# Kernel optimization log

Hardware: AMD Instinct MI355X
Metric: run time of the kernel (lower is better)

The kernel has to match this reference:

```python
import jax, jax.numpy as jnp
import numpy as np

# ---- config (matches init_kwargs) ----
M, N, D = 8, 512, 243            # meshes, neurons per mesh, input dim
E_RATIO = 0.8
NE = int(N * E_RATIO)            # 409 excitatory
NI = N - NE                      # 103 inhibitory
TICKS = 16
BATCH = 512
BITS = 4
WSCALE = 8.0
VTH, VRESET = 1.0, 0.0
TAU_E, TAU_I, DT = 2.0, 1.5, 1.0
BETA = 10.0                      # fast-sigmoid surrogate slope
INPUT_SCALE = 1.0


def fake_quant(w):
    """Quantization-aware fake quant with straight-through estimator."""
    step = WSCALE / (2 ** (BITS - 1))          # 1.0 for 4-bit, scale 8
    q = jnp.clip(jnp.round(w / step), -(2 ** (BITS - 1)), 2 ** (BITS - 1) - 1) * step
    return w + jax.lax.stop_gradient(q - w)


@jax.custom_vjp
def spike(u):
    return (u >= 0.0).astype(u.dtype)

def _spike_fwd(u):
    return spike(u), u

def _spike_bwd(u, g):
    # fast-sigmoid surrogate gradient
    return (g * BETA / (1.0 + BETA * jnp.abs(u)) ** 2,)

spike.defvjp(_spike_fwd, _spike_bwd)


def setup_inputs() -> dict:
    key = jax.random.key(0)
    ks = jax.random.split(key, 8)

    def sparse_w(k, shape, density, std, zero_diag=False):
        km, kw = jax.random.split(k)
        mask = (jax.random.uniform(km, shape) < density).astype(jnp.float32)
        if zero_diag:
            mask = mask * (1.0 - jnp.eye(shape[-1], dtype=jnp.float32))
        return jax.random.normal(kw, shape) * std * mask

    x = jax.random.normal(ks[0], (BATCH, D), dtype=jnp.float32)
    W_in = jax.random.normal(ks[1], (M, N, D)) * 0.8      # per-mesh input projection [out,in]
    b_in = jax.random.normal(ks[2], (M, N)) * 0.05
    W_inter = sparse_w(ks[3], (M, N, NE), 0.3, 0.8)        # inter-mesh: E of mesh m -> mesh m+1
    W_EE = sparse_w(ks[4], (M, NE, NE), 0.5, 0.8, True)
    W_EI = sparse_w(ks[5], (M, NI, NE), 0.6, 0.8)
    W_IE = sparse_w(ks[6], (M, NE, NI), 0.8, 0.8)
    W_II = sparse_w(ks[7], (M, NI, NI), 0.7, 0.8, True)
    return dict(x=x, W_in=W_in, b_in=b_in, W_inter=W_inter,
                W_EE=W_EE, W_EI=W_EI, W_IE=W_IE, W_II=W_II)


def reference(x, W_in, b_in, W_inter, W_EE, W_EI, W_IE, W_II):
    B = x.shape[0]
    decay_E = 1.0 - DT / TAU_E
    decay_I = 1.0 - DT / TAU_I

    # quantize weights once (constant across ticks)
    qW_in, qW_inter = fake_quant(W_in), fake_quant(W_inter)
    qW_EE, qW_EI = fake_quant(W_EE), fake_quant(W_EI)
    qW_IE, qW_II = fake_quant(W_IE), fake_quant(W_II)

    # external input projection, same every tick: [M, B, N]
    ext_proj = jnp.einsum('bd,mnd->mbn', x * INPUT_SCALE, qW_in) + b_in[:, None, :]

    def tick(carry, _):
        e, i, vE, vI, acc = carry          # e:[M,B,NE] i:[M,B,NI]
        # inter-mesh: mesh m receives inter_connections[m-1](e_prev[m-1])
        inter = jnp.einsum('mbe,mne->mbn', e, qW_inter)
        ext = ext_proj + jnp.roll(inter, 1, axis=0)
        cE = ext[:, :, :NE] \
            + jnp.einsum('mbe,mfe->mbf', e, qW_EE) \
            + jnp.einsum('mbi,mfi->mbf', i, qW_IE)
        cI = ext[:, :, NE:] \
            + jnp.einsum('mbe,mfe->mbf', e, qW_EI) \
            + jnp.einsum('mbi,mfi->mbf', i, qW_II)
        # LIF: leaky decay + input, threshold, hard reset
        vE = vE * decay_E + cE * DT
        vI = vI * decay_I + cI * DT
        sE = spike(vE - VTH)
        sI = spike(vI - VTH)
        vE = sE * VRESET + (1.0 - sE) * vE
        vI = sI * VRESET + (1.0 - sI) * vI
        acc = acc + jnp.concatenate([sE, sI], axis=-1)
        return (sE, sI, vE, vI, acc), None

    z = jnp.zeros
    carry0 = (z((M, B, NE)), z((M, B, NI)), z((M, B, NE)), z((M, B, NI)), z((M, B, N)))
    (eF, iF, vEF, vIF, acc), _ = jax.lax.scan(tick, carry0, None, length=TICKS)
    # accumulator laid out mesh-major: [B, M*N]
    return jnp.transpose(acc, (1, 0, 2)).reshape(B, M * N)
```

## Files before the change

kernel.cpp:

```cpp
#include <hip/hip_runtime.h>
#include <hip/hip_bf16.h>

#define Mm 8
#define Nn 512
#define NEe 409
#define NIi 103
#define Bb 512
#define Dd 243
#define Tt 16
#define SPROW 640
#define WCROW 1152
#define DEC_I 0.33333334f
#define NBLK 256
#define FLAGSTRIDE 16
#define SPINMAX 1000000L

typedef int v4i __attribute__((ext_vector_type(4)));
union LV { long l[2]; v4i v; };

__device__ __forceinline__ float quantf(float w) {
    float q = rintf(w);
    return fminf(fmaxf(q, -8.0f), 7.0f);
}

__global__ void k_pack(const float* __restrict__ Wint, const float* __restrict__ WEE,
                       const float* __restrict__ WEI, const float* __restrict__ WIE,
                       const float* __restrict__ WII, signed char* __restrict__ Wc) {
    int q = blockIdx.x * 256 + threadIdx.x;
    if (q >= (Mm * Nn * WCROW) / 4) return;
    int k0 = (q * 4) % WCROW;
    int n  = ((q * 4) / WCROW) & (Nn - 1);
    int m  = (q * 4) / (WCROW * Nn);
    char out4[4];
#pragma unroll
    for (int j = 0; j < 4; ++j) {
        int k = k0 + j;
        float w = 0.0f;
        if (k < 512) {
            if (k < NEe) w = Wint[((((m + 7) & 7) * Nn) + n) * NEe + k];
        } else if (k < 1024) {
            int jj = k - 512;
            if (jj < NEe) w = (n < NEe) ? WEE[((m * NEe) + n) * NEe + jj]
                                        : WEI[((m * NIi) + (n - NEe)) * NEe + jj];
        } else {
            int jj = k - 1024;
            if (jj < NIi) w = (n < NEe) ? WIE[((m * NEe) + n) * NIi + jj]
                                        : WII[((m * NIi) + (n - NEe)) * NIi + jj];
        }
        out4[j] = (signed char)(int)quantf(w);
    }
    *(int*)&Wc[q * 4] = *(int*)out4;
}

__global__ void k_ext(const float* __restrict__ x, const float* __restrict__ Win,
                      const float* __restrict__ bin, float* __restrict__ ext) {
    __shared__ float xs[64][68];
    __shared__ float wsm[64][68];
    const int bid = blockIdx.x;
    const int m  = bid >> 6;
    const int bt = (bid >> 3) & 7;
    const int nt = bid & 7;
    const int b0 = bt * 64, n0 = nt * 64;
    const int t = threadIdx.x;
    const int tb4 = (t & 15) * 4;
    const int tn4 = (t >> 4) * 4;
    const int sr = t >> 2;
    const int sc = (t & 3) * 16;
    float c[4][4];
#pragma unroll
    for (int i = 0; i < 4; ++i)
#pragma unroll
        for (int j = 0; j < 4; ++j) c[i][j] = 0.0f;

    for (int d0 = 0; d0 < Dd; d0 += 64) {
#pragma unroll
        for (int j = 0; j < 16; ++j) {
            int d = d0 + sc + j;
            float xv = 0.0f, wv = 0.0f;
            if (d < Dd) {
                xv = x[(b0 + sr) * Dd + d];
                wv = quantf(Win[((m * Nn) + n0 + sr) * Dd + d]);
            }
            xs[sc + j][sr] = xv;
            wsm[sc + j][sr] = wv;
        }
        __syncthreads();
        const int dmax = min(64, Dd - d0);
        for (int d = 0; d < dmax; ++d) {
            float4 av = *(const float4*)&xs[d][tb4];
            float4 wv = *(const float4*)&wsm[d][tn4];
            float a[4] = {av.x, av.y, av.z, av.w};
            float wq[4] = {wv.x, wv.y, wv.z, wv.w};
#pragma unroll
            for (int i = 0; i < 4; ++i)
#pragma unroll
                for (int j = 0; j < 4; ++j)
                    c[i][j] = fmaf(a[i], wq[j], c[i][j]);
        }
        __syncthreads();
    }
#pragma unroll
    for (int i = 0; i < 4; ++i)
#pragma unroll
        for (int j = 0; j < 4; ++j) {
            float val = __fadd_rn(c[i][j], bin[m * Nn + n0 + tn4 + j]);
            ext[(size_t)(m * Bb + b0 + tb4 + i) * Nn + n0 + tn4 + j] = val;
        }
}

__global__ void __launch_bounds__(512, 2)
k_ticks(const signed char* __restrict__ Wc,
        signed char* __restrict__ Sp0,
        signed char* __restrict__ Sp1,
        const float* __restrict__ ext,
        float* __restrict__ out,
        int* __restrict__ flags) {
    __shared__ __align__(16) signed char sA[2][64][256];
    __shared__ __align__(16) signed char sB[2][128][256];

    const int wg = blockIdx.x;
    const int m  = wg & 7;
    const int bt = (wg >> 3) & 7;
    const int nt = wg >> 6;
    const int b0 = bt * 64;
    const int n0 = nt * 128;
    const int pm = (m + 7) & 7;
    const int nm = (m + 1) & 7;

    const int tid  = threadIdx.x;
    const int w    = tid >> 6;
    const int lane = tid & 63;
    const int bh   = w & 1;
    const int nh   = w >> 1;
    const int quad = lane >> 4;
    const int li   = lane & 15;

    int waitIdx = 0;
    if (tid < 12) {
        int g  = tid >> 2;
        int mm = (g == 0) ? pm : ((g == 1) ? m : nm);
        waitIdx = (((tid & 3) << 6) | (bt << 3) | mm) * FLAGSTRIDE;
    }

    int rowA[2], cnkA[2], gcolA[2], scolA[2];
#pragma unroll
    for (int j = 0; j < 2; ++j) {
        int ch = tid + j * 512;
        rowA[j]  = ch >> 4;
        cnkA[j]  = ch & 15;
        gcolA[j] = cnkA[j] * 16;
        scolA[j] = (cnkA[j] ^ (rowA[j] & 15)) * 16;
    }
    int rowB[4], cnkB[4], gcolB[4], scolB[4];
#pragma unroll
    for (int j = 0; j < 4; ++j) {
        int ch = tid + j * 512;
        rowB[j]  = ch >> 4;
        cnkB[j]  = ch & 15;
        gcolB[j] = cnkB[j] * 16;
        scolB[j] = (cnkB[j] ^ (rowB[j] & 15)) * 16;
    }

    float decs[2]; int offs[2]; int nels[2];
#pragma unroll
    for (int tn = 0; tn < 2; ++tn) {
        int n = n0 + nh * 32 + tn * 16 + li;
        nels[tn] = n;
        decs[tn] = (n < NEe) ? 0.5f : DEC_I;
        offs[tn] = (n < NEe) ? n : (n + 103);
    }
    const int bbase = b0 + bh * 32;

    const signed char* WcBase = Wc + (size_t)(m * Nn + n0) * WCROW;

    float extr[2][2][4];
#pragma unroll
    for (int tb = 0; tb < 2; ++tb)
#pragma unroll
        for (int tn = 0; tn < 2; ++tn)
#pragma unroll
            for (int r = 0; r < 4; ++r) {
                int b = bbase + tb * 16 + quad * 4 + r;
                extr[tb][tn][r] = ext[(size_t)(m * Bb + b) * Nn + nels[tn]];
            }
    float vmem[2][2][4];
    int cnt[2][2];
#pragma unroll
    for (int tb = 0; tb < 2; ++tb)
#pragma unroll
        for (int tn = 0; tn < 2; ++tn) {
            cnt[tb][tn] = 0;
#pragma unroll
            for (int r = 0; r < 4; ++r) vmem[tb][tn][r] = 0.0f;
        }

    if (nt == 0) {
        for (int idx = tid; idx < 64 * 128 * 2; idx += 512) {
            int bufsel = idx >> 13;
            int rr = (idx >> 7) & 63;
            int p  = idx & 127;
            int off = (p < 103) ? (409 + p) : (615 + (p - 103));
            signed char* base = (bufsel ? Sp1 : Sp0) + (size_t)(m * Bb + b0 + rr) * SPROW + off;
            __hip_atomic_store(base, (signed char)0, __ATOMIC_RELAXED, __HIP_MEMORY_SCOPE_AGENT);
        }
    }

    for (int t = 0; t < Tt; ++t) {
        signed char* SR = (t & 1) ? Sp1 : Sp0;
        signed char* SW = (t & 1) ? Sp0 : Sp1;
        signed char* AbasePrev = SR + (size_t)(pm * Bb + b0) * SPROW;
        signed char* AbaseOwn  = SR + (size_t)(m  * Bb + b0) * SPROW;

        if (t > 0) {
            if (tid < 12) {
                long spin = 0;
                while (__hip_atomic_load(&flags[waitIdx],
                                         __ATOMIC_RELAXED, __HIP_MEMORY_SCOPE_AGENT) < t) {
                    __builtin_amdgcn_s_sleep(2);
                    if (++spin > SPINMAX) break;
                }
            }
            __syncthreads();
        }

        float c[2][2][4];

        if (t == 0) {
#pragma unroll
            for (int tb = 0; tb < 2; ++tb)
#pragma unroll
                for (int tn = 0; tn < 2; ++tn)
#pragma unroll
                    for (int r = 0; r < 4; ++r)
                        c[tb][tn][r] = __fadd_rn(__fadd_rn(__fadd_rn(extr[tb][tn][r], 0.0f), 0.0f), 0.0f);
        } else {
            v4i acc[2][2];
#pragma unroll
            for (int tb = 0; tb < 2; ++tb)
#pragma unroll
                for (int tn = 0; tn < 2; ++tn) acc[tb][tn] = (v4i){0, 0, 0, 0};

#pragma unroll
            for (int j = 0; j < 2; ++j) {
                long* ap = (long*)(AbasePrev + (size_t)rowA[j] * SPROW + gcolA[j]);
                LV tmp;
                tmp.l[0] = __hip_atomic_load(ap,     __ATOMIC_RELAXED, __HIP_MEMORY_SCOPE_AGENT);
                tmp.l[1] = __hip_atomic_load(ap + 1, __ATOMIC_RELAXED, __HIP_MEMORY_SCOPE_AGENT);
                *(v4i*)&sA[0][rowA[j]][scolA[j]] = tmp.v;
            }
#pragma unroll
            for (int j = 0; j < 4; ++j)
                *(v4i*)&sB[0][rowB[j]][scolB[j]] =
                    *(const v4i*)(WcBase + (size_t)rowB[j] * WCROW + gcolB[j]);
            __syncthreads();

            for (int it = 0; it < 4; ++it) {
                const int buf = it & 1;
                const int k0 = (it + 1) * 256;
                signed char* ab; int ko;
                if (k0 < 512) { ab = AbasePrev; ko = k0; }
                else          { ab = AbaseOwn;  ko = k0 - 512; }
                const int kw = (it == 3) ? 128 : 256;
                v4i nA[2], nB[4];
                bool ldA[2], ldB[4];
#pragma unroll
                for (int j = 0; j < 2; ++j) {
                    ldA[j] = (gcolA[j] < kw);
                    if (ldA[j]) {
                        long* ap = (long*)(ab + (size_t)rowA[j] * SPROW + ko + gcolA[j]);
                        LV tmp;
                        tmp.l[0] = __hip_atomic_load(ap,     __ATOMIC_RELAXED, __HIP_MEMORY_SCOPE_AGENT);
                        tmp.l[1] = __hip_atomic_load(ap + 1, __ATOMIC_RELAXED, __HIP_MEMORY_SCOPE_AGENT);
                        nA[j] = tmp.v;
                    }
                }
#pragma unroll
                for (int j = 0; j < 4; ++j) {
                    ldB[j] = (gcolB[j] < kw);
                    if (ldB[j])
                        nB[j] = *(const v4i*)(WcBase + (size_t)rowB[j] * WCROW + k0 + gcolB[j]);
                }
#pragma unroll
                for (int ks = 0; ks < 256; ks += 64) {
                    const int c0 = (((ks >> 4) + quad) ^ li) * 16;
                    v4i af0 = *(const v4i*)&sA[buf][bh * 32 + li][c0];
                    v4i af1 = *(const v4i*)&sA[buf][bh * 32 + 16 + li][c0];
#pragma unroll
                    for (int tn = 0; tn < 2; ++tn) {
                        v4i bfr = *(const v4i*)&sB[buf][nh * 32 + tn * 16 + li][c0];
                        acc[0][tn] = __builtin_amdgcn_mfma_i32_16x16x64_i8(af0, bfr, acc[0][tn], 0, 0, 0);
                        acc[1][tn] = __builtin_amdgcn_mfma_i32_16x16x64_i8(af1, bfr, acc[1][tn], 0, 0, 0);
                    }
                }
                const int nb = buf ^ 1;
#pragma unroll
                for (int j = 0; j < 2; ++j)
                    if (ldA[j]) *(v4i*)&sA[nb][rowA[j]][scolA[j]] = nA[j];
#pragma unroll
                for (int j = 0; j < 4; ++j)
                    if (ldB[j]) *(v4i*)&sB[nb][rowB[j]][scolB[j]] = nB[j];
                __syncthreads();
                if (it == 1) {
#pragma unroll
                    for (int tb = 0; tb < 2; ++tb)
#pragma unroll
                        for (int tn = 0; tn < 2; ++tn) {
#pragma unroll
                            for (int r = 0; r < 4; ++r)
                                c[tb][tn][r] = __fadd_rn(extr[tb][tn][r], (float)acc[tb][tn][r]);
                            acc[tb][tn] = (v4i){0, 0, 0, 0};
                        }
                } else if (it == 3) {
#pragma unroll
                    for (int tb = 0; tb < 2; ++tb)
#pragma unroll
                        for (int tn = 0; tn < 2; ++tn) {
#pragma unroll
                            for (int r = 0; r < 4; ++r)
                                c[tb][tn][r] = __fadd_rn(c[tb][tn][r], (float)acc[tb][tn][r]);
                            acc[tb][tn] = (v4i){0, 0, 0, 0};
                        }
                }
            }
#pragma unroll
            for (int ks = 0; ks < 128; ks += 64) {
                const int c0 = (((ks >> 4) + quad) ^ li) * 16;
                v4i af0 = *(const v4i*)&sA[0][bh * 32 + li][c0];
                v4i af1 = *(const v4i*)&sA[0][bh * 32 + 16 + li][c0];
#pragma unroll
                for (int tn = 0; tn < 2; ++tn) {
                    v4i bfr = *(const v4i*)&sB[0][nh * 32 + tn * 16 + li][c0];
                    acc[0][tn] = __builtin_amdgcn_mfma_i32_16x16x64_i8(af0, bfr, acc[0][tn], 0, 0, 0);
                    acc[1][tn] = __builtin_amdgcn_mfma_i32_16x16x64_i8(af1, bfr, acc[1][tn], 0, 0, 0);
                }
            }
#pragma unroll
            for (int tb = 0; tb < 2; ++tb)
#pragma unroll
                for (int tn = 0; tn < 2; ++tn)
#pragma unroll
                    for (int r = 0; r < 4; ++r)
                        c[tb][tn][r] = __fadd_rn(c[tb][tn][r], (float)acc[tb][tn][r]);
        }

#pragma unroll
        for (int tb = 0; tb < 2; ++tb)
#pragma unroll
            for (int tn = 0; tn < 2; ++tn)
#pragma unroll
                for (int r = 0; r < 4; ++r) {
                    float vn = __fadd_rn(__fmul_rn(vmem[tb][tn][r], decs[tn]), c[tb][tn][r]);
                    int s = (vn >= 1.0f) ? 1 : 0;
                    vmem[tb][tn][r] = s ? 0.0f : vn;
                    cnt[tb][tn] += s << (r * 8);
                    if (t < Tt - 1) {
                        int b = bbase + tb * 16 + quad * 4 + r;
                        signed char* sp = SW + (size_t)(m * Bb + b) * SPROW + offs[tn];
                        __hip_atomic_store(sp, (signed char)s,
                                           __ATOMIC_RELAXED, __HIP_MEMORY_SCOPE_AGENT);
                    }
                }
        if (t < Tt - 1) {
            __syncthreads();
            if (tid == 0)
                __hip_atomic_store(&flags[wg * FLAGSTRIDE], t + 1,
                                   __ATOMIC_RELAXED, __HIP_MEMORY_SCOPE_AGENT);
        }
    }

#pragma unroll
    for (int tb = 0; tb < 2; ++tb)
#pragma unroll
        for (int tn = 0; tn < 2; ++tn)
#pragma unroll
            for (int r = 0; r < 4; ++r) {
                int b = bbase + tb * 16 + quad * 4 + r;
                out[(size_t)b * (Mm * Nn) + m * Nn + nels[tn]] =
                    (float)((cnt[tb][tn] >> (r * 8)) & 0xff);
            }
}

extern "C" void kernel_launch(void* const* d_in, const int* in_sizes, int n_in,
                              void* d_out, int out_size, void* d_ws, size_t ws_size,
                              hipStream_t stream) {
    const float* x    = (const float*)d_in[0];
    const float* Win  = (const float*)d_in[1];
    const float* bin  = (const float*)d_in[2];
    const float* Wint = (const float*)d_in[3];
    const float* WEE  = (const float*)d_in[4];
    const float* WEI  = (const float*)d_in[5];
    const float* WIE  = (const float*)d_in[6];
    const float* WII  = (const float*)d_in[7];
    float* out = (float*)d_out;

    char* ws = (char*)d_ws;
    signed char* Wc  = (signed char*)ws;
    signed char* Sp0 = (signed char*)(ws + 4718592);
    signed char* Sp1 = Sp0 + 2621440;
    int* flags = (int*)(ws + 4718592 + 2 * 2621440);
    float* extw = (float*)(ws + 4718592 + 2 * 2621440 + 32768);

    k_pack<<<(Mm * Nn * WCROW / 4 + 255) / 256, 256, 0, stream>>>(Wint, WEE, WEI, WIE, WII, Wc);
    k_ext<<<512, 256, 0, stream>>>(x, Win, bin, extw);
    k_ticks<<<NBLK, 512, 0, stream>>>(Wc, Sp0, Sp1, (const float*)extw, out, flags);
}
```

Baseline: 226.3 us.

## Fuse weight packing and input projection into the persistent tick kernel

Removes the separate k_pack and k_ext launches. Each tick workgroup now computes its own 64x128 tile of the input projection in shared memory and keeps it in registers. It also quantizes and packs its int8 weight tile during the first matmul tick (t==1), writing it to global memory for reuse in later ticks. This cuts two launches and the round trip of ext through global memory, but puts the pack and projection work on the critical path of the persistent kernel. It also raises shared memory use to 96KB, which may affect the two-blocks-per-CU occupancy.

```diff
diff --git a/kernel.cpp b/kernel.cpp
--- a/kernel.cpp
+++ b/kernel.cpp
@@ -23,21 +23,19 @@
     return fminf(fmaxf(q, -8.0f), 7.0f);
 }
 
-__global__ void k_pack(const float* __restrict__ Wint, const float* __restrict__ WEE,
-                       const float* __restrict__ WEI, const float* __restrict__ WIE,
-                       const float* __restrict__ WII, signed char* __restrict__ Wc) {
-    int q = blockIdx.x * 256 + threadIdx.x;
-    if (q >= (Mm * Nn * WCROW) / 4) return;
-    int k0 = (q * 4) % WCROW;
-    int n  = ((q * 4) / WCROW) & (Nn - 1);
-    int m  = (q * 4) / (WCROW * Nn);
-    char out4[4];
-#pragma unroll
-    for (int j = 0; j < 4; ++j) {
-        int k = k0 + j;
+__device__ __forceinline__ v4i packW16(const float* __restrict__ Wint,
+                                       const float* __restrict__ WEE,
+                                       const float* __restrict__ WEI,
+                                       const float* __restrict__ WIE,
+                                       const float* __restrict__ WII,
+                                       int m, int pm, int n, int k0) {
+    union { signed char b[16]; v4i v; } u;
+#pragma unroll
+    for (int e = 0; e < 16; ++e) {
+        int k = k0 + e;
         float w = 0.0f;
         if (k < 512) {
-            if (k < NEe) w = Wint[((((m + 7) & 7) * Nn) + n) * NEe + k];
+            if (k < NEe) w = Wint[((pm * Nn) + n) * NEe + k];
         } else if (k < 1024) {
             int jj = k - 512;
             if (jj < NEe) w = (n < NEe) ? WEE[((m * NEe) + n) * NEe + jj]
@@ -47,76 +45,29 @@
             if (jj < NIi) w = (n < NEe) ? WIE[((m * NEe) + n) * NIi + jj]
                                         : WII[((m * NIi) + (n - NEe)) * NIi + jj];
         }
-        out4[j] = (signed char)(int)quantf(w);
-    }
-    *(int*)&Wc[q * 4] = *(int*)out4;
+        u.b[e] = (signed char)(int)quantf(w);
+    }
+    return u.v;
 }
 
-__global__ void k_ext(const float* __restrict__ x, const float* __restrict__ Win,
-                      const float* __restrict__ bin, float* __restrict__ ext) {
-    __shared__ float xs[64][68];
-    __shared__ float wsm[64][68];
-    const int bid = blockIdx.x;
-    const int m  = bid >> 6;
-    const int bt = (bid >> 3) & 7;
-    const int nt = bid & 7;
-    const int b0 = bt * 64, n0 = nt * 64;
-    const int t = threadIdx.x;
-    const int tb4 = (t & 15) * 4;
-    const int tn4 = (t >> 4) * 4;
-    const int sr = t >> 2;
-    const int sc = (t & 3) * 16;
-    float c[4][4];
-#pragma unroll
-    for (int i = 0; i < 4; ++i)
-#pragma unroll
-        for (int j = 0; j < 4; ++j) c[i][j] = 0.0f;
-
-    for (int d0 = 0; d0 < Dd; d0 += 64) {
-#pragma unroll
-        for (int j = 0; j < 16; ++j) {
-            int d = d0 + sc + j;
-            float xv = 0.0f, wv = 0.0f;
-            if (d < Dd) {
-                xv = x[(b0 + sr) * Dd + d];
-                wv = quantf(Win[((m * Nn) + n0 + sr) * Dd + d]);
-            }
-            xs[sc + j][sr] = xv;
-            wsm[sc + j][sr] = wv;
-        }
-        __syncthreads();
-        const int dmax = min(64, Dd - d0);
-        for (int d = 0; d < dmax; ++d) {
-            float4 av = *(const float4*)&xs[d][tb4];
-            float4 wv = *(const float4*)&wsm[d][tn4];
-            float a[4] = {av.x, av.y, av.z, av.w};
-            float wq[4] = {wv.x, wv.y, wv.z, wv.w};
-#pragma unroll
-            for (int i = 0; i < 4; ++i)
-#pragma unroll
-                for (int j = 0; j < 4; ++j)
-                    c[i][j] = fmaf(a[i], wq[j], c[i][j]);
-        }
-        __syncthreads();
-    }
-#pragma unroll
-    for (int i = 0; i < 4; ++i)
-#pragma unroll
-        for (int j = 0; j < 4; ++j) {
-            float val = __fadd_rn(c[i][j], bin[m * Nn + n0 + tn4 + j]);
-            ext[(size_t)(m * Bb + b0 + tb4 + i) * Nn + n0 + tn4 + j] = val;
-        }
-}
-
 __global__ void __launch_bounds__(512, 2)
-k_ticks(const signed char* __restrict__ Wc,
+k_ticks(const float* __restrict__ Wint, const float* __restrict__ WEE,
+        const float* __restrict__ WEI, const float* __restrict__ WIE,
+        const float* __restrict__ WII,
+        signed char* __restrict__ Wc,
         signed char* __restrict__ Sp0,
         signed char* __restrict__ Sp1,
-        const float* __restrict__ ext,
+        const float* __restrict__ x,
+        const float* __restrict__ Win,
+        const float* __restrict__ bin,
         float* __restrict__ out,
         int* __restrict__ flags) {
-    __shared__ __align__(16) signed char sA[2][64][256];
-    __shared__ __align__(16) signed char sB[2][128][256];
+    __shared__ __align__(16) char smem[98304];
+    float (*xs)[68]   = (float (*)[68])smem;
+    float (*wsm)[132] = (float (*)[132])(smem + 17408);
+    float (*et)[132]  = (float (*)[132])(smem + 51200);
+    signed char (*sA)[64][256]  = (signed char (*)[64][256])smem;
+    signed char (*sB)[128][256] = (signed char (*)[128][256])(smem + 32768);
 
     const int wg = blockIdx.x;
     const int m  = wg & 7;
@@ -142,23 +93,23 @@
         waitIdx = (((tid & 3) << 6) | (bt << 3) | mm) * FLAGSTRIDE;
     }
 
-    int rowA[2], cnkA[2], gcolA[2], scolA[2];
+    int rowA[2], gcolA[2], scolA[2];
 #pragma unroll
     for (int j = 0; j < 2; ++j) {
         int ch = tid + j * 512;
         rowA[j]  = ch >> 4;
-        cnkA[j]  = ch & 15;
-        gcolA[j] = cnkA[j] * 16;
-        scolA[j] = (cnkA[j] ^ (rowA[j] & 15)) * 16;
-    }
-    int rowB[4], cnkB[4], gcolB[4], scolB[4];
+        int cnk  = ch & 15;
+        gcolA[j] = cnk * 16;
+        scolA[j] = (cnk ^ (rowA[j] & 15)) * 16;
+    }
+    int rowB[4], gcolB[4], scolB[4];
 #pragma unroll
     for (int j = 0; j < 4; ++j) {
         int ch = tid + j * 512;
         rowB[j]  = ch >> 4;
-        cnkB[j]  = ch & 15;
-        gcolB[j] = cnkB[j] * 16;
-        scolB[j] = (cnkB[j] ^ (rowB[j] & 15)) * 16;
+        int cnk  = ch & 15;
+        gcolB[j] = cnk * 16;
+        scolB[j] = (cnk ^ (rowB[j] & 15)) * 16;
     }
 
     float decs[2]; int offs[2]; int nels[2];
@@ -170,19 +121,64 @@
         offs[tn] = (n < NEe) ? n : (n + 103);
     }
     const int bbase = b0 + bh * 32;
-
-    const signed char* WcBase = Wc + (size_t)(m * Nn + n0) * WCROW;
+    signed char* WcBase = Wc + (size_t)(m * Nn + n0) * WCROW;
 
     float extr[2][2][4];
-#pragma unroll
-    for (int tb = 0; tb < 2; ++tb)
-#pragma unroll
-        for (int tn = 0; tn < 2; ++tn)
-#pragma unroll
-            for (int r = 0; r < 4; ++r) {
-                int b = bbase + tb * 16 + quad * 4 + r;
-                extr[tb][tn][r] = ext[(size_t)(m * Bb + b) * Nn + nels[tn]];
-            }
+    {
+        const int tb4 = (tid & 15) * 4;
+        const int tn4 = (tid >> 4) * 4;
+        const int sr  = tid & 63;
+        const int sc  = (tid >> 6) * 8;
+        const int wr  = tid & 127;
+        const int wc2 = (tid >> 7) * 16;
+        float c4[4][4];
+#pragma unroll
+        for (int i = 0; i < 4; ++i)
+#pragma unroll
+            for (int j = 0; j < 4; ++j) c4[i][j] = 0.0f;
+
+        for (int d0 = 0; d0 < Dd; d0 += 64) {
+#pragma unroll
+            for (int j = 0; j < 8; ++j) {
+                int d = d0 + sc + j;
+                xs[sc + j][sr] = (d < Dd) ? x[(b0 + sr) * Dd + d] : 0.0f;
+            }
+#pragma unroll
+            for (int j = 0; j < 16; ++j) {
+                int d = d0 + wc2 + j;
+                wsm[wc2 + j][wr] = (d < Dd) ? quantf(Win[((m * Nn) + n0 + wr) * Dd + d]) : 0.0f;
+            }
+            __syncthreads();
+            const int dmax = min(64, Dd - d0);
+            for (int d = 0; d < dmax; ++d) {
+                float4 av = *(const float4*)&xs[d][tb4];
+                float4 wv = *(const float4*)&wsm[d][tn4];
+                float a[4] = {av.x, av.y, av.z, av.w};
+                float wq[4] = {wv.x, wv.y, wv.z, wv.w};
+#pragma unroll
+                for (int i = 0; i < 4; ++i)
+#pragma unroll
+                    for (int j = 0; j < 4; ++j)
+                        c4[i][j] = fmaf(a[i], wq[j], c4[i][j]);
+            }
+            __syncthreads();
+        }
+#pragma unroll
+        for (int i = 0; i < 4; ++i)
+#pragma unroll
+            for (int j = 0; j < 4; ++j)
+                et[tb4 + i][tn4 + j] = __fadd_rn(c4[i][j], bin[m * Nn + n0 + tn4 + j]);
+        __syncthreads();
+#pragma unroll
+        for (int tb = 0; tb < 2; ++tb)
+#pragma unroll
+            for (int tn = 0; tn < 2; ++tn)
+#pragma unroll
+                for (int r = 0; r < 4; ++r)
+                    extr[tb][tn][r] = et[bh * 32 + tb * 16 + quad * 4 + r][nh * 32 + tn * 16 + li];
+        __syncthreads();
+    }
+
     float vmem[2][2][4];
     int cnt[2][2];
 #pragma unroll
@@ -248,10 +244,19 @@
                 tmp.l[1] = __hip_atomic_load(ap + 1, __ATOMIC_RELAXED, __HIP_MEMORY_SCOPE_AGENT);
                 *(v4i*)&sA[0][rowA[j]][scolA[j]] = tmp.v;
             }
-#pragma unroll
-            for (int j = 0; j < 4; ++j)
-                *(v4i*)&sB[0][rowB[j]][scolB[j]] =
-                    *(const v4i*)(WcBase + (size_t)rowB[j] * WCROW + gcolB[j]);
+            if (t == 1) {
+#pragma unroll
+                for (int j = 0; j < 4; ++j) {
+                    v4i pw = packW16(Wint, WEE, WEI, WIE, WII, m, pm, n0 + rowB[j], gcolB[j]);
+                    *(v4i*)&WcBase[(size_t)rowB[j] * WCROW + gcolB[j]] = pw;
+                    *(v4i*)&sB[0][rowB[j]][scolB[j]] = pw;
+                }
+            } else {
+#pragma unroll
+                for (int j = 0; j < 4; ++j)
+                    *(v4i*)&sB[0][rowB[j]][scolB[j]] =
+                        *(const v4i*)(WcBase + (size_t)rowB[j] * WCROW + gcolB[j]);
+            }
             __syncthreads();
 
             for (int it = 0; it < 4; ++it) {
@@ -277,8 +282,15 @@
 #pragma unroll
                 for (int j = 0; j < 4; ++j) {
                     ldB[j] = (gcolB[j] < kw);
-                    if (ldB[j])
-                        nB[j] = *(const v4i*)(WcBase + (size_t)rowB[j] * WCROW + k0 + gcolB[j]);
+                    if (ldB[j]) {
+                        if (t == 1) {
+                            nB[j] = packW16(Wint, WEE, WEI, WIE, WII, m, pm,
+                                            n0 + rowB[j], k0 + gcolB[j]);
+                            *(v4i*)&WcBase[(size_t)rowB[j] * WCROW + k0 + gcolB[j]] = nB[j];
+                        } else {
+                            nB[j] = *(const v4i*)(WcBase + (size_t)rowB[j] * WCROW + k0 + gcolB[j]);
+                        }
+                    }
                 }
 #pragma unroll
                 for (int ks = 0; ks < 256; ks += 64) {
@@ -398,9 +410,7 @@
     signed char* Sp0 = (signed char*)(ws + 4718592);
     signed char* Sp1 = Sp0 + 2621440;
     int* flags = (int*)(ws + 4718592 + 2 * 2621440);
-    float* extw = (float*)(ws + 4718592 + 2 * 2621440 + 32768);
-
-    k_pack<<<(Mm * Nn * WCROW / 4 + 255) / 256, 256, 0, stream>>>(Wint, WEE, WEI, WIE, WII, Wc);
-    k_ext<<<512, 256, 0, stream>>>(x, Win, bin, extw);
-    k_ticks<<<NBLK, 512, 0, stream>>>(Wc, Sp0, Sp1, (const float*)extw, out, flags);
+
+    k_ticks<<<NBLK, 512, 0, stream>>>(Wint, WEE, WEI, WIE, WII,
+                                      Wc, Sp0, Sp1, x, Win, bin, out, flags);
 }
```

Result: slower. 326.3 us (+44.2%).
